# Kernel optimization log

Measured on AMD Instinct MI355X. Metric: run time of the kernel, lower is better.

## Reference

```python
import jax, jax.numpy as jnp
import numpy as np


def setup_inputs() -> dict:
    key = jax.random.key(0)
    k1, k2 = jax.random.split(key)
    B, C, H, L = 4, 1, 1024, 4096
    x = jax.random.normal(k1, (B, H, L), dtype=jnp.float32)
    k = jax.random.normal(k2, (C, H, L), dtype=jnp.float32)
    return {"x": x, "k": k}


def reference(x, k):
    # x: (B, H, L) input; k: (C, H, l_kernel) SSM convolution kernel.
    # FFT convolution with zero-padding to n = l_kernel + L (linear conv),
    # then truncate to the first L outputs (causal conv output).
    L = x.shape[-1]
    l_kernel = k.shape[-1]
    n = l_kernel + L
    k_f = jnp.fft.rfft(k, n=n)                       # (C, H, n//2+1) complex
    x_f = jnp.fft.rfft(x, n=n)                       # (B, H, n//2+1) complex
    y_f = jnp.einsum('bhl,chl->bchl', x_f, k_f)      # broadcast complex multiply
    y = jnp.fft.irfft(y_f, n=n)[..., :L]             # (B, C, H, L)
    return y
```

## Files before the change

kernel.cpp:

```cpp
#include <hip/hip_runtime.h>

#define THREADS 256
#define B_DIM   4
#define H_DIM   1024
#define L_DIM   4096
#define NFFT    4096
#define PI_F     3.14159265358979323846f
#define TWO_PI_F 6.28318530717958647692f

__device__ __forceinline__ float2 cmulf(float2 a, float2 b) {
    return make_float2(a.x*b.x - a.y*b.y, a.x*b.y + a.y*b.x);
}
__device__ __forceinline__ float2 caddf(float2 a, float2 b){ return make_float2(a.x+b.x, a.y+b.y); }
__device__ __forceinline__ float2 csubf(float2 a, float2 b){ return make_float2(a.x-b.x, a.y-b.y); }

__device__ __forceinline__ int swz(int i) { return i ^ ((i>>4)&15) ^ ((i>>8)&15); }

__device__ __forceinline__ int drev12(int x) {
    return ((x & 15) << 8) | (x & 0xF0) | (x >> 8);
}

__device__ __forceinline__ void make_tw(float base, float2 w[16]) {
    float sn, cs; __sincosf(base, &sn, &cs);
    w[1]  = make_float2(cs, sn);
    w[2]  = cmulf(w[1], w[1]);
    w[3]  = cmulf(w[2], w[1]);
    w[4]  = cmulf(w[2], w[2]);
    w[5]  = cmulf(w[4], w[1]);
    w[6]  = cmulf(w[4], w[2]);
    w[7]  = cmulf(w[4], w[3]);
    w[8]  = cmulf(w[4], w[4]);
    w[9]  = cmulf(w[8], w[1]);
    w[10] = cmulf(w[8], w[2]);
    w[11] = cmulf(w[8], w[3]);
    w[12] = cmulf(w[8], w[4]);
    w[13] = cmulf(w[8], w[5]);
    w[14] = cmulf(w[8], w[6]);
    w[15] = cmulf(w[8], w[7]);
}

__device__ __forceinline__ float2 w16c(int q, float s) {
    constexpr float C[8] = {1.f, 0.9238795325f, 0.7071067812f, 0.3826834324f,
                            0.f, -0.3826834324f, -0.7071067812f, -0.9238795325f};
    constexpr float S[8] = {0.f, 0.3826834324f, 0.7071067812f, 0.9238795325f,
                            1.f, 0.9238795325f, 0.7071067812f, 0.3826834324f};
    return make_float2(C[q], s*S[q]);
}

template<int SGN>
__device__ __forceinline__ float2 twq(float2 d, int q) {
    if (q == 0) return d;
    if (q == 4) return make_float2((float)(-SGN)*d.y, (float)SGN*d.x);
    return cmulf(d, w16c(q, (float)SGN));
}

template<int SGN, bool HZ>
__device__ __forceinline__ void dif16(float2 v[16]) {
    if (HZ) {
        #pragma unroll
        for (int i = 0; i < 8; ++i) {
            float2 a = v[i];
            v[i+8] = twq<SGN>(a, i);
        }
    } else {
        #pragma unroll
        for (int i = 0; i < 8; ++i) {
            float2 a = v[i], b = v[i+8];
            v[i]   = caddf(a,b);
            v[i+8] = twq<SGN>(csubf(a,b), i);
        }
    }
    #pragma unroll
    for (int h = 4; h >= 1; h >>= 1) {
        const int step = 8 / h;
        #pragma unroll
        for (int g = 0; g < 16; g += 2*h) {
            #pragma unroll
            for (int i = 0; i < h; ++i) {
                float2 a = v[g+i], b = v[g+i+h];
                v[g+i]   = caddf(a,b);
                v[g+i+h] = twq<SGN>(csubf(a,b), i*step);
            }
        }
    }
}

template<int SGN>
__device__ __forceinline__ void dit16(float2 v[16]) {
    #pragma unroll
    for (int h = 1; h <= 8; h <<= 1) {
        const int step = 8 / h;
        #pragma unroll
        for (int g = 0; g < 16; g += 2*h) {
            #pragma unroll
            for (int i = 0; i < h; ++i) {
                float2 a = v[g+i];
                float2 b = twq<SGN>(v[g+i+h], i*step);
                v[g+i]   = caddf(a,b);
                v[g+i+h] = csubf(a,b);
            }
        }
    }
}

__device__ __forceinline__ void fwd_fft_12(const float2* __restrict__ src, float2* Z, int t) {
    constexpr int REV4[16] = {0,8,4,12,2,10,6,14,1,9,5,13,3,11,7,15};
    float2 v[16], w[16];
    #pragma unroll
    for (int r = 0; r < 8; ++r) v[r] = src[256*r + t];
    dif16<-1, true>(v);
    make_tw(-TWO_PI_F * (float)t / (float)NFFT, w);
    #pragma unroll
    for (int kk = 1; kk < 16; ++kk) v[REV4[kk]] = cmulf(v[REV4[kk]], w[kk]);
    #pragma unroll
    for (int kk = 0; kk < 16; ++kk) Z[swz(256*kk + t)] = v[REV4[kk]];
    __syncthreads();

    const int k1 = t >> 4, m = t & 15;
    const int rb = 256*k1 + m;
    #pragma unroll
    for (int r = 0; r < 16; ++r) v[r] = Z[swz(rb + 16*r)];
    dif16<-1,false>(v);
    make_tw(-TWO_PI_F * (float)m / 256.f, w);
    #pragma unroll
    for (int kk = 1; kk < 16; ++kk) v[REV4[kk]] = cmulf(v[REV4[kk]], w[kk]);
    #pragma unroll
    for (int kk = 0; kk < 16; ++kk) Z[swz(rb + 16*kk)] = v[REV4[kk]];
    __syncthreads();
}

__device__ __forceinline__ void fwd_fft_row(const float2* __restrict__ src, float2* Z, int t) {
    constexpr int REV4[16] = {0,8,4,12,2,10,6,14,1,9,5,13,3,11,7,15};
    fwd_fft_12(src, Z, t);
    float2 v[16];
    const int b3 = t << 4;
    #pragma unroll
    for (int r = 0; r < 16; ++r) v[r] = Z[swz(b3 + r)];
    dif16<-1,false>(v);
    #pragma unroll
    for (int kk = 0; kk < 16; ++kk) Z[swz(b3 + kk)] = v[REV4[kk]];
}

__device__ __forceinline__ int binpos(int j) {
    return swz( ((j&15)<<8) | (((j>>4)&15)<<4) | (j>>8) );
}


__global__ __launch_bounds__(THREADS, 3)
void kpq_kernel(const float* __restrict__ k, float4* __restrict__ PQ_all) {
    __shared__ float2 Zk[NFFT];
    constexpr int REV4[16] = {0,8,4,12,2,10,6,14,1,9,5,13,3,11,7,15};
    const int t  = threadIdx.x;
    const int hh = blockIdx.x;
    const float2* kp = (const float2*)(k + (size_t)hh * L_DIM);

    fwd_fft_12(kp, Zk, t);

    const int b3 = t << 4;
    float2 v[16];
    #pragma unroll
    for (int r = 0; r < 16; ++r) v[r] = Zk[swz(b3 + r)];
    dif16<-1,false>(v);
    #pragma unroll
    for (int kk = 0; kk < 16; ++kk) Zk[swz(b3 + kk)] = v[REV4[kk]];
    __syncthreads();

    const int j1 = t & 15, j0 = t >> 4;
    const int rdig = (j1 << 4) | j0;
    const int C = t ? drev12(NFFT - rdig) : 16;
    const int M = t ? (NFFT - 1) : 15;

    float4* PQh = PQ_all + (size_t)hh * NFFT;
    const float sc = 1.f / (float)NFFT;

    #pragma unroll
    for (int kk = 0; kk < 16; ++kk) {
        float2 Zj = v[REV4[kk]];
        float2 zm = Zk[swz((C - kk) & M)];
        float2 Zmc = make_float2(zm.x, -zm.y);

        int j = (kk << 8) | rdig;
        float sn, cs; __sincosf(-PI_F * (float)j / (float)NFFT, &sn, &cs);
        const float c = cs, d = sn;
        float2 u1 = make_float2(1.f + d, -c);
        float2 u2 = make_float2(1.f - d,  c);
        float2 A   = caddf(cmulf(u1, Zj), cmulf(u2, Zmc));
        float2 Amc = caddf(cmulf(u2, Zj), cmulf(u1, Zmc));
        float2 P = make_float2(0.25f*((1.f+d)*A.x + (1.f-d)*Amc.x),
                               0.25f*((1.f+d)*A.y + (1.f-d)*Amc.y));
        float2 dK = csubf(A, Amc);
        float2 Q = make_float2(-0.25f*c*dK.y, 0.25f*c*dK.x);
        PQh[(kk << 8) | t] = make_float4(P.x*sc, P.y*sc, Q.x*sc, Q.y*sc);
    }
}

__global__ __launch_bounds__(THREADS, 3)
void conv_pq_kernel(const float* __restrict__ x, const float4* __restrict__ PQ_all,
                    float* __restrict__ out) {
    __shared__ float2 Zx[NFFT];
    constexpr int REV4[16] = {0,8,4,12,2,10,6,14,1,9,5,13,3,11,7,15};

    const int t  = threadIdx.x;
    const int wg = blockIdx.x;
    const int hh = wg & (H_DIM - 1);
    const int b  = wg >> 10;

    const float2* xp = (const float2*)(x + ((size_t)(b*H_DIM + hh)) * L_DIM);

    fwd_fft_12(xp, Zx, t);

    const float4* PQh = PQ_all + (size_t)hh * NFFT;
    float4 pq[16];
    #pragma unroll
    for (int kk = 0; kk < 16; ++kk) pq[kk] = PQh[(kk << 8) | t];

    const int b3 = t << 4;
    float2 v[16];
    #pragma unroll
    for (int r = 0; r < 16; ++r) v[r] = Zx[swz(b3 + r)];
    dif16<-1,false>(v);
    #pragma unroll
    for (int kk = 0; kk < 16; ++kk) Zx[swz(b3 + kk)] = v[REV4[kk]];
    __syncthreads();

    const int j1 = t & 15, j0 = t >> 4;
    const int rdig = (j1 << 4) | j0;
    const int C = t ? drev12(NFFT - rdig) : 16;
    const int M = t ? (NFFT - 1) : 15;

    float2 vy[16];
    #pragma unroll
    for (int kk = 0; kk < 16; ++kk) {
        float2 Zj = v[REV4[kk]];
        float2 zm = Zx[swz((C - kk) & M)];
        float2 P = make_float2(pq[kk].x, pq[kk].y);
        float2 Q = make_float2(pq[kk].z, pq[kk].w);
        float2 r1 = cmulf(P, Zj);
        float2 r2 = make_float2(Q.x*zm.x + Q.y*zm.y, Q.y*zm.x - Q.x*zm.y);
        vy[REV4[kk]] = caddf(r1, r2);
    }
    dit16<1>(vy);
    __syncthreads();
    #pragma unroll
    for (int mm = 0; mm < 16; ++mm) Zx[swz(b3 + mm)] = vy[mm];
    __syncthreads();

    float2 vx[16], w[16];
    const int k1 = t >> 4, m = t & 15;
    const int rb = 256*k1 + m;
    make_tw(TWO_PI_F * (float)m / 256.f, w);
    #pragma unroll
    for (int kk = 0; kk < 16; ++kk) {
        float2 val = Zx[swz(rb + 16*kk)];
        if (kk > 0) val = cmulf(val, w[kk]);
        vx[REV4[kk]] = val;
    }
    dit16<1>(vx);
    #pragma unroll
    for (int r = 0; r < 16; ++r) Zx[swz(rb + 16*r)] = vx[r];
    __syncthreads();

    make_tw(TWO_PI_F * (float)t / (float)NFFT, w);
    #pragma unroll
    for (int kk = 0; kk < 16; ++kk) {
        float2 val = Zx[swz(256*kk + t)];
        if (kk > 0) val = cmulf(val, w[kk]);
        vx[REV4[kk]] = val;
    }
    dit16<1>(vx);
    float2* op = (float2*)(out + ((size_t)(b*H_DIM + hh)) * L_DIM);
    #pragma unroll
    for (int n1 = 0; n1 < 8; ++n1) {
        op[256*n1 + t] = vx[n1];
    }
}

__global__ __launch_bounds__(THREADS, 4)
void kfft_kernel(const float* __restrict__ k, float2* __restrict__ Kf_all) {
    __shared__ float2 Zk[NFFT];
    const int t  = threadIdx.x;
    const int hh = blockIdx.x;
    const float2* kp = (const float2*)(k + (size_t)hh * L_DIM);

    fwd_fft_row(kp, Zk, t);
    __syncthreads();

    float2* Kf = Kf_all + (size_t)hh * NFFT;
    #pragma unroll
    for (int s = 0; s < 8; ++s) {
        int j = t + 256*s;
        if (j == 0) {
            float2 zk = Zk[0];
            Kf[0] = make_float2(zk.x + zk.y, zk.x - zk.y);
            float2 zk2 = Zk[swz(8)];
            Kf[2048] = make_float2(zk2.x, -zk2.y);
        } else {
            int jm = NFFT - j;
            float2 zkj = Zk[binpos(j)], zkm = Zk[binpos(jm)];
            float sn, cs; __sincosf(-PI_F * (float)j / (float)NFFT, &sn, &cs);
            float2 w = make_float2(cs, sn);
            float2 Ke = make_float2(0.5f*(zkj.x + zkm.x), 0.5f*(zkj.y - zkm.y));
            float2 dk = make_float2(zkj.x - zkm.x, zkj.y + zkm.y);
            float2 Ko = make_float2(0.5f*dk.y, -0.5f*dk.x);
            float2 tk = cmulf(w, Ko);
            Kf[j]  = caddf(Ke, tk);
            Kf[jm] = make_float2(Ke.x - tk.x, -(Ke.y - tk.y));
        }
    }
}

__global__ __launch_bounds__(THREADS, 4)
void conv_main_kernel(const float* __restrict__ x, const float2* __restrict__ Kf_all,
                      float* __restrict__ out) {
    __shared__ float2 Zx[NFFT];
    constexpr int REV4[16] = {0,8,4,12,2,10,6,14,1,9,5,13,3,11,7,15};

    const int t  = threadIdx.x;
    const int wg = blockIdx.x;
    const int hh = wg & (H_DIM - 1);
    const int b  = wg >> 10;

    const float2* xp = (const float2*)(x + ((size_t)(b*H_DIM + hh)) * L_DIM);
    const float2* Kf = Kf_all + (size_t)hh * NFFT;

    fwd_fft_row(xp, Zx, t);

    float2 kfj[8], kfm[8], kf2;
    #pragma unroll
    for (int s = 0; s < 8; ++s) {
        int j = t + 256*s;
        kfj[s] = Kf[j];
        kfm[s] = Kf[(NFFT - j) & (NFFT - 1)];
    }
    kf2 = Kf[2048];
    __syncthreads();

    #pragma unroll
    for (int s = 0; s < 8; ++s) {
        int j = t + 256*s;
        if (j == 0) {
            float2 zx = Zx[0];
            float ax0 = zx.x + zx.y, axM = zx.x - zx.y;
            float y0 = ax0 * kfj[0].x, yM = axM * kfj[0].y;
            Zx[0] = make_float2(0.5f*(y0 + yM), 0.5f*(y0 - yM));
            int p2 = swz(8);
            float2 zx2 = Zx[p2];
            Zx[p2] = cmulf(zx2, make_float2(kf2.x, -kf2.y));
        } else {
            int jm = NFFT - j;
            int pj = binpos(j), pm = binpos(jm);
            float2 zxj = Zx[pj], zxm = Zx[pm];

            float sn, cs; __sincosf(-PI_F * (float)j / (float)NFFT, &sn, &cs);
            float2 w = make_float2(cs, sn);

            float2 Xe = make_float2(0.5f*(zxj.x + zxm.x), 0.5f*(zxj.y - zxm.y));
            float2 dx = make_float2(zxj.x - zxm.x, zxj.y + zxm.y);
            float2 Xo = make_float2(0.5f*dx.y, -0.5f*dx.x);
            float2 tx = cmulf(w, Xo);
            float2 Axj = caddf(Xe, tx);
            float2 Axm = make_float2(Xe.x - tx.x, -(Xe.y - tx.y));

            float2 Yj = cmulf(Axj, kfj[s]);
            float2 Ym = cmulf(Axm, kfm[s]);

            float2 u  = make_float2(0.5f*(Yj.x + Ym.x), 0.5f*(Yj.y - Ym.y));
            float2 dd = make_float2(Yj.x - Ym.x, Yj.y + Ym.y);
            float2 wc = make_float2(w.x, -w.y);
            float2 vv = cmulf(wc, dd);
            vv.x *= 0.5f; vv.y *= 0.5f;
            Zx[pj] = make_float2(u.x - vv.y, u.y + vv.x);
            Zx[pm] = make_float2(u.x + vv.y, -(u.y - vv.x));
        }
    }
    __syncthreads();

    float2 vx[16], w[16];
    const int k1 = t >> 4, m = t & 15;
    const int rb = 256*k1 + m;
    const int b3 = t << 4;

    #pragma unroll
    for (int r = 0; r < 16; ++r) vx[REV4[r]] = Zx[swz(b3 + r)];
    dit16<1>(vx);
    #pragma unroll
    for (int mm = 0; mm < 16; ++mm) Zx[swz(b3 + mm)] = vx[mm];
    __syncthreads();

    make_tw(TWO_PI_F * (float)m / 256.f, w);
    #pragma unroll
    for (int kk = 0; kk < 16; ++kk) {
        float2 val = Zx[swz(rb + 16*kk)];
        if (kk > 0) val = cmulf(val, w[kk]);
        vx[REV4[kk]] = val;
    }
    dit16<1>(vx);
    #pragma unroll
    for (int r = 0; r < 16; ++r) Zx[swz(rb + 16*r)] = vx[r];
    __syncthreads();

    make_tw(TWO_PI_F * (float)t / (float)NFFT, w);
    #pragma unroll
    for (int kk = 0; kk < 16; ++kk) {
        float2 val = Zx[swz(256*kk + t)];
        if (kk > 0) val = cmulf(val, w[kk]);
        vx[REV4[kk]] = val;
    }
    dit16<1>(vx);
    float2* op = (float2*)(out + ((size_t)(b*H_DIM + hh)) * L_DIM);
    const float sc = 1.f / (float)NFFT;
    #pragma unroll
    for (int n1 = 0; n1 < 8; ++n1) {
        float2 z = vx[n1];
        op[256*n1 + t] = make_float2(z.x*sc, z.y*sc);
    }
}

__global__ __launch_bounds__(THREADS, 2)
void fftconv_fallback(const float* __restrict__ x, const float* __restrict__ k,
                      float* __restrict__ out) {
    __shared__ float2 Zx[NFFT];
    __shared__ float2 Zk[NFFT];
    constexpr int REV4[16] = {0,8,4,12,2,10,6,14,1,9,5,13,3,11,7,15};

    const int t  = threadIdx.x;
    const int wg = blockIdx.x;
    const int hh = wg & (H_DIM - 1);
    const int b  = wg >> 10;

    const float2* xp = (const float2*)(x + ((size_t)(b*H_DIM + hh)) * L_DIM);
    const float2* kp = (const float2*)(k + (size_t)hh * L_DIM);

    fwd_fft_row(xp, Zx, t);
    __syncthreads();
    fwd_fft_row(kp, Zk, t);
    __syncthreads();

    #pragma unroll
    for (int s = 0; s < 8; ++s) {
        int j = t + 256*s;
        if (j == 0) {
            float2 zx = Zx[0], zk = Zk[0];
            float ax0 = zx.x + zx.y, axM = zx.x - zx.y;
            float ak0 = zk.x + zk.y, akM = zk.x - zk.y;
            float y0 = ax0*ak0, yM = axM*akM;
            Zx[0] = make_float2(0.5f*(y0+yM), 0.5f*(y0-yM));
            int p2 = swz(8);
            Zx[p2] = cmulf(Zx[p2], Zk[p2]);
        } else {
            int jm = NFFT - j;
            int pj = binpos(j), pm = binpos(jm);
            float2 zxj = Zx[pj], zxm = Zx[pm];
            float2 zkj = Zk[pj], zkm = Zk[pm];
            float sn, cs; __sincosf(-PI_F * (float)j / (float)NFFT, &sn, &cs);
            float2 w = make_float2(cs, sn);
            float2 Xe = make_float2(0.5f*(zxj.x + zxm.x), 0.5f*(zxj.y - zxm.y));
            float2 dx = make_float2(zxj.x - zxm.x, zxj.y + zxm.y);
            float2 Xo = make_float2(0.5f*dx.y, -0.5f*dx.x);
            float2 tx = cmulf(w, Xo);
            float2 Axj = caddf(Xe, tx);
            float2 Axm = make_float2(Xe.x - tx.x, -(Xe.y - tx.y));
            float2 Ke = make_float2(0.5f*(zkj.x + zkm.x), 0.5f*(zkj.y - zkm.y));
            float2 dk = make_float2(zkj.x - zkm.x, zkj.y + zkm.y);
            float2 Ko = make_float2(0.5f*dk.y, -0.5f*dk.x);
            float2 tk = cmulf(w, Ko);
            float2 Akj = caddf(Ke, tk);
            float2 Akm = make_float2(Ke.x - tk.x, -(Ke.y - tk.y));
            float2 Yj = cmulf(Axj, Akj);
            float2 Ym = cmulf(Axm, Akm);
            float2 u  = make_float2(0.5f*(Yj.x + Ym.x), 0.5f*(Yj.y - Ym.y));
            float2 dd = make_float2(Yj.x - Ym.x, Yj.y + Ym.y);
            float2 wc = make_float2(w.x, -w.y);
            float2 vv = cmulf(wc, dd);
            vv.x *= 0.5f; vv.y *= 0.5f;
            Zx[pj] = make_float2(u.x - vv.y, u.y + vv.x);
            Zx[pm] = make_float2(u.x + vv.y, -(u.y - vv.x));
        }
    }
    __syncthreads();

    float2 vx[16], w[16];
    const int k1 = t >> 4, m = t & 15;
    const int rb = 256*k1 + m;
    const int b3 = t << 4;

    #pragma unroll
    for (int r = 0; r < 16; ++r) vx[REV4[r]] = Zx[swz(b3 + r)];
    dit16<1>(vx);
    #pragma unroll
    for (int mm = 0; mm < 16; ++mm) Zx[swz(b3 + mm)] = vx[mm];
    __syncthreads();

    make_tw(TWO_PI_F * (float)m / 256.f, w);
    #pragma unroll
    for (int kk = 0; kk < 16; ++kk) {
        float2 val = Zx[swz(rb + 16*kk)];
        if (kk > 0) val = cmulf(val, w[kk]);
        vx[REV4[kk]] = val;
    }
    dit16<1>(vx);
    #pragma unroll
    for (int r = 0; r < 16; ++r) Zx[swz(rb + 16*r)] = vx[r];
    __syncthreads();

    make_tw(TWO_PI_F * (float)t / (float)NFFT, w);
    #pragma unroll
    for (int kk = 0; kk < 16; ++kk) {
        float2 val = Zx[swz(256*kk + t)];
        if (kk > 0) val = cmulf(val, w[kk]);
        vx[REV4[kk]] = val;
    }
    dit16<1>(vx);
    float2* op = (float2*)(out + ((size_t)(b*H_DIM + hh)) * L_DIM);
    const float sc = 1.f / (float)NFFT;
    #pragma unroll
    for (int n1 = 0; n1 < 8; ++n1) {
        float2 z = vx[n1];
        op[256*n1 + t] = make_float2(z.x*sc, z.y*sc);
    }
}

extern "C" void kernel_launch(void* const* d_in, const int* in_sizes, int n_in,
                              void* d_out, int out_size, void* d_ws, size_t ws_size,
                              hipStream_t stream) {
    const float* x = (const float*)d_in[0];
    const float* k = (const float*)d_in[1];
    float* out = (float*)d_out;
    const size_t needPQ = (size_t)H_DIM * NFFT * sizeof(float4);
    const size_t needKf = (size_t)H_DIM * NFFT * sizeof(float2);
    if (ws_size >= needPQ) {
        float4* PQ = (float4*)d_ws;
        kpq_kernel<<<dim3(H_DIM), dim3(THREADS), 0, stream>>>(k, PQ);
        conv_pq_kernel<<<dim3(B_DIM * H_DIM), dim3(THREADS), 0, stream>>>(x, PQ, out);
    } else if (ws_size >= needKf) {
        float2* Kf = (float2*)d_ws;
        kfft_kernel<<<dim3(H_DIM), dim3(THREADS), 0, stream>>>(k, Kf);
        conv_main_kernel<<<dim3(B_DIM * H_DIM), dim3(THREADS), 0, stream>>>(x, Kf, out);
    } else {
        fftconv_fallback<<<dim3(B_DIM * H_DIM), dim3(THREADS), 0, stream>>>(x, k, out);
    }
}
```

Measured before the change: 183.0 us.

## Process two batch rows per workgroup to share kernel spectrum loads

```diff
diff --git a/kernel.cpp b/kernel.cpp
--- a/kernel.cpp
+++ b/kernel.cpp
@@ -194,33 +194,85 @@
     }
 }
 
-__global__ __launch_bounds__(THREADS, 3)
-void conv_pq_kernel(const float* __restrict__ x, const float4* __restrict__ PQ_all,
-                    float* __restrict__ out) {
-    __shared__ float2 Zx[NFFT];
+__global__ __launch_bounds__(THREADS, 2)
+void conv_pq2_kernel(const float* __restrict__ x, const float4* __restrict__ PQ_all,
+                     float* __restrict__ out) {
+    __shared__ float2 Z0[NFFT];
+    __shared__ float2 Z1[NFFT];
     constexpr int REV4[16] = {0,8,4,12,2,10,6,14,1,9,5,13,3,11,7,15};
 
     const int t  = threadIdx.x;
     const int wg = blockIdx.x;
     const int hh = wg & (H_DIM - 1);
-    const int b  = wg >> 10;
-
-    const float2* xp = (const float2*)(x + ((size_t)(b*H_DIM + hh)) * L_DIM);
-
-    fwd_fft_12(xp, Zx, t);
+    const int bp = wg >> 10;
+    const int b0 = bp * 2, b1 = bp * 2 + 1;
+
+    const float2* xp0 = (const float2*)(x + ((size_t)(b0*H_DIM + hh)) * L_DIM);
+    const float2* xp1 = (const float2*)(x + ((size_t)(b1*H_DIM + hh)) * L_DIM);
+
+    float2 v0[16], v1[16], w[16];
+
+    #pragma unroll
+    for (int r = 0; r < 8; ++r) v0[r] = xp0[256*r + t];
+    #pragma unroll
+    for (int r = 0; r < 8; ++r) v1[r] = xp1[256*r + t];
+    dif16<-1, true>(v0);
+    dif16<-1, true>(v1);
+    make_tw(-TWO_PI_F * (float)t / (float)NFFT, w);
+    #pragma unroll
+    for (int kk = 1; kk < 16; ++kk) {
+        v0[REV4[kk]] = cmulf(v0[REV4[kk]], w[kk]);
+        v1[REV4[kk]] = cmulf(v1[REV4[kk]], w[kk]);
+    }
+    #pragma unroll
+    for (int kk = 0; kk < 16; ++kk) {
+        int p = swz(256*kk + t);
+        Z0[p] = v0[REV4[kk]];
+        Z1[p] = v1[REV4[kk]];
+    }
+    __syncthreads();
+
+    const int k1 = t >> 4, m = t & 15;
+    const int rb = 256*k1 + m;
+    #pragma unroll
+    for (int r = 0; r < 16; ++r) v0[r] = Z0[swz(rb + 16*r)];
+    #pragma unroll
+    for (int r = 0; r < 16; ++r) v1[r] = Z1[swz(rb + 16*r)];
+    dif16<-1,false>(v0);
+    dif16<-1,false>(v1);
+    make_tw(-TWO_PI_F * (float)m / 256.f, w);
+    #pragma unroll
+    for (int kk = 1; kk < 16; ++kk) {
+        v0[REV4[kk]] = cmulf(v0[REV4[kk]], w[kk]);
+        v1[REV4[kk]] = cmulf(v1[REV4[kk]], w[kk]);
+    }
+    #pragma unroll
+    for (int kk = 0; kk < 16; ++kk) {
+        int p = swz(rb + 16*kk);
+        Z0[p] = v0[REV4[kk]];
+        Z1[p] = v1[REV4[kk]];
+    }
+    __syncthreads();
+
+    const int b3 = t << 4;
+    #pragma unroll
+    for (int r = 0; r < 16; ++r) v0[r] = Z0[swz(b3 + r)];
+    #pragma unroll
+    for (int r = 0; r < 16; ++r) v1[r] = Z1[swz(b3 + r)];
+    dif16<-1,false>(v0);
+    dif16<-1,false>(v1);
 
     const float4* PQh = PQ_all + (size_t)hh * NFFT;
     float4 pq[16];
     #pragma unroll
     for (int kk = 0; kk < 16; ++kk) pq[kk] = PQh[(kk << 8) | t];
 
-    const int b3 = t << 4;
-    float2 v[16];
-    #pragma unroll
-    for (int r = 0; r < 16; ++r) v[r] = Zx[swz(b3 + r)];
-    dif16<-1,false>(v);
-    #pragma unroll
-    for (int kk = 0; kk < 16; ++kk) Zx[swz(b3 + kk)] = v[REV4[kk]];
+    #pragma unroll
+    for (int kk = 0; kk < 16; ++kk) {
+        int p = swz(b3 + kk);
+        Z0[p] = v0[REV4[kk]];
+        Z1[p] = v1[REV4[kk]];
+    }
     __syncthreads();
 
     const int j1 = t & 15, j0 = t >> 4;
@@ -228,51 +280,83 @@
     const int C = t ? drev12(NFFT - rdig) : 16;
     const int M = t ? (NFFT - 1) : 15;
 
-    float2 vy[16];
-    #pragma unroll
-    for (int kk = 0; kk < 16; ++kk) {
-        float2 Zj = v[REV4[kk]];
-        float2 zm = Zx[swz((C - kk) & M)];
+    float2 vy0[16];
+    #pragma unroll
+    for (int kk = 0; kk < 16; ++kk) {
+        float2 Zj = v0[REV4[kk]];
+        float2 zm = Z0[swz((C - kk) & M)];
         float2 P = make_float2(pq[kk].x, pq[kk].y);
         float2 Q = make_float2(pq[kk].z, pq[kk].w);
         float2 r1 = cmulf(P, Zj);
         float2 r2 = make_float2(Q.x*zm.x + Q.y*zm.y, Q.y*zm.x - Q.x*zm.y);
-        vy[REV4[kk]] = caddf(r1, r2);
-    }
-    dit16<1>(vy);
-    __syncthreads();
-    #pragma unroll
-    for (int mm = 0; mm < 16; ++mm) Zx[swz(b3 + mm)] = vy[mm];
-    __syncthreads();
-
-    float2 vx[16], w[16];
-    const int k1 = t >> 4, m = t & 15;
-    const int rb = 256*k1 + m;
+        vy0[REV4[kk]] = caddf(r1, r2);
+    }
+    dit16<1>(vy0);
+
+    float2 vy1[16];
+    #pragma unroll
+    for (int kk = 0; kk < 16; ++kk) {
+        float2 Zj = v1[REV4[kk]];
+        float2 zm = Z1[swz((C - kk) & M)];
+        float2 P = make_float2(pq[kk].x, pq[kk].y);
+        float2 Q = make_float2(pq[kk].z, pq[kk].w);
+        float2 r1 = cmulf(P, Zj);
+        float2 r2 = make_float2(Q.x*zm.x + Q.y*zm.y, Q.y*zm.x - Q.x*zm.y);
+        vy1[REV4[kk]] = caddf(r1, r2);
+    }
+    dit16<1>(vy1);
+    __syncthreads();
+    #pragma unroll
+    for (int mm = 0; mm < 16; ++mm) {
+        int p = swz(b3 + mm);
+        Z0[p] = vy0[mm];
+        Z1[p] = vy1[mm];
+    }
+    __syncthreads();
+
     make_tw(TWO_PI_F * (float)m / 256.f, w);
-    #pragma unroll
-    for (int kk = 0; kk < 16; ++kk) {
-        float2 val = Zx[swz(rb + 16*kk)];
-        if (kk > 0) val = cmulf(val, w[kk]);
-        vx[REV4[kk]] = val;
-    }
-    dit16<1>(vx);
-    #pragma unroll
-    for (int r = 0; r < 16; ++r) Zx[swz(rb + 16*r)] = vx[r];
+    float2 vx[16];
+    #pragma unroll
+    for (int kk = 0; kk < 16; ++kk) {
+        float2 val = Z0[swz(rb + 16*kk)];
+        if (kk > 0) val = cmulf(val, w[kk]);
+        vx[REV4[kk]] = val;
+    }
+    dit16<1>(vx);
+    #pragma unroll
+    for (int r = 0; r < 16; ++r) Z0[swz(rb + 16*r)] = vx[r];
+    #pragma unroll
+    for (int kk = 0; kk < 16; ++kk) {
+        float2 val = Z1[swz(rb + 16*kk)];
+        if (kk > 0) val = cmulf(val, w[kk]);
+        vx[REV4[kk]] = val;
+    }
+    dit16<1>(vx);
+    #pragma unroll
+    for (int r = 0; r < 16; ++r) Z1[swz(rb + 16*r)] = vx[r];
     __syncthreads();
 
     make_tw(TWO_PI_F * (float)t / (float)NFFT, w);
-    #pragma unroll
-    for (int kk = 0; kk < 16; ++kk) {
-        float2 val = Zx[swz(256*kk + t)];
-        if (kk > 0) val = cmulf(val, w[kk]);
-        vx[REV4[kk]] = val;
-    }
-    dit16<1>(vx);
-    float2* op = (float2*)(out + ((size_t)(b*H_DIM + hh)) * L_DIM);
-    #pragma unroll
-    for (int n1 = 0; n1 < 8; ++n1) {
-        op[256*n1 + t] = vx[n1];
-    }
+    float2* op0 = (float2*)(out + ((size_t)(b0*H_DIM + hh)) * L_DIM);
+    float2* op1 = (float2*)(out + ((size_t)(b1*H_DIM + hh)) * L_DIM);
+    #pragma unroll
+    for (int kk = 0; kk < 16; ++kk) {
+        float2 val = Z0[swz(256*kk + t)];
+        if (kk > 0) val = cmulf(val, w[kk]);
+        vx[REV4[kk]] = val;
+    }
+    dit16<1>(vx);
+    #pragma unroll
+    for (int n1 = 0; n1 < 8; ++n1) op0[256*n1 + t] = vx[n1];
+    #pragma unroll
+    for (int kk = 0; kk < 16; ++kk) {
+        float2 val = Z1[swz(256*kk + t)];
+        if (kk > 0) val = cmulf(val, w[kk]);
+        vx[REV4[kk]] = val;
+    }
+    dit16<1>(vx);
+    #pragma unroll
+    for (int n1 = 0; n1 < 8; ++n1) op1[256*n1 + t] = vx[n1];
 }
 
 __global__ __launch_bounds__(THREADS, 4)
@@ -531,7 +615,7 @@
     if (ws_size >= needPQ) {
         float4* PQ = (float4*)d_ws;
         kpq_kernel<<<dim3(H_DIM), dim3(THREADS), 0, stream>>>(k, PQ);
-        conv_pq_kernel<<<dim3(B_DIM * H_DIM), dim3(THREADS), 0, stream>>>(x, PQ, out);
+        conv_pq2_kernel<<<dim3(B_DIM * H_DIM / 2), dim3(THREADS), 0, stream>>>(x, PQ, out);
     } else if (ws_size >= needKf) {
         float2* Kf = (float2*)d_ws;
         kfft_kernel<<<dim3(H_DIM), dim3(THREADS), 0, stream>>>(k, Kf);
```

New measurement: 222.9 us. 21.8% more time.
